# Optimization experiments

Hardware: AMD Instinct MI355X
Metric: run time of the kernel (lower is better)

## Reference

```python
import jax, jax.numpy as jnp
import numpy as np
from jax import lax

DN = ('NCHW', 'OIHW', 'NCHW')

def _conv(x, k, stride):
    return lax.conv_general_dilated(x, k, (stride, stride), 'VALID', dimension_numbers=DN)

def setup_inputs() -> dict:
    key = jax.random.key(0)
    ks = jax.random.split(key, 20)
    B, E, A, D = 2048, 8, 6, 64 * 7 * 7  # batch, rm_states, actions, flat conv dim (3136)
    s = 0.05
    inp = {
        'state': jax.random.normal(ks[0], (B, 84, 84, 3), jnp.float32),
        'rm_state': jax.random.randint(ks[1], (B,), 0, E, jnp.int64),
        # conv encoder params
        'k1': jax.random.normal(ks[2], (32, 3, 8, 8), jnp.float32) * s,
        'c1': jnp.zeros((32,), jnp.float32),
        'k2': jax.random.normal(ks[3], (64, 32, 4, 4), jnp.float32) * s,
        'c2': jnp.zeros((64,), jnp.float32),
        'k3': jax.random.normal(ks[4], (64, 64, 3, 3), jnp.float32) * s,
        'c3': jnp.zeros((64,), jnp.float32),
        # stacked per-rm-state expert MLP params (E experts)
        'W1': jax.random.normal(ks[5], (E, D, 64), jnp.float32) * s,
        'B1': jnp.zeros((E, 64), jnp.float32),
        'W2': jax.random.normal(ks[6], (E, 64, 64), jnp.float32) * s,
        'B2': jnp.zeros((E, 64), jnp.float32),
        'W3': jax.random.normal(ks[7], (E, 64, 64), jnp.float32) * s,
        'B3': jnp.zeros((E, 64), jnp.float32),
        'W4': jax.random.normal(ks[8], (E, 64, 64), jnp.float32) * s,
        'B4': jnp.zeros((E, 64), jnp.float32),
        'W5': jax.random.normal(ks[9], (E, 64, 64), jnp.float32) * s,
        'B5': jnp.zeros((E, 64), jnp.float32),
        'W6': jax.random.normal(ks[10], (E, 64, A), jnp.float32) * s,
        'B6': jnp.zeros((E, A), jnp.float32),
    }
    return inp

def reference(state, rm_state, k1, c1, k2, c2, k3, c3,
              W1, B1, W2, B2, W3, B3, W4, B4, W5, B5, W6, B6):
    # NHWC -> NCHW (matches torch's view-based channel-first rearrangement intent)
    x = jnp.transpose(state, (0, 3, 1, 2))
    x = jax.nn.relu(_conv(x, k1, 4) + c1[None, :, None, None])
    x = jax.nn.relu(_conv(x, k2, 2) + c2[None, :, None, None])
    x = jax.nn.relu(_conv(x, k3, 1) + c3[None, :, None, None])
    B = x.shape[0]
    flat = x.reshape(B, -1)                              # [B, 3136]
    # batched expert MLPs: compute all experts, then gather per-sample expert output
    h = jax.nn.relu(jnp.einsum('bd,edh->ebh', flat, W1) + B1[:, None, :])  # [E,B,64]
    for W, Bb in ((W2, B2), (W3, B3), (W4, B4), (W5, B5)):
        h = jax.nn.relu(jnp.einsum('ebh,ehk->ebk', h, W) + Bb[:, None, :])
    out = jnp.einsum('ebh,eha->eba', h, W6) + B6[:, None, :]               # [E,B,A]
    return out[rm_state, jnp.arange(B)]                  # [B, A]
```

## Files before the change

kernel.cpp:

```cpp
#include <hip/hip_runtime.h>

#define BATCH 2048

typedef unsigned short u16;
typedef __attribute__((ext_vector_type(8))) short bf16x8;
typedef __attribute__((ext_vector_type(4))) float f32x4;

static __device__ __forceinline__ float b2f(u16 h) {
  union { unsigned u; float f; } x; x.u = ((unsigned)h) << 16; return x.f;
}
static __device__ __forceinline__ u16 f2b(float f) {
  union { float f; unsigned u; } x; x.f = f;
  return (u16)((x.u + 0x7fffu + ((x.u >> 16) & 1u)) >> 16);
}
static __device__ __forceinline__ void split2(float v, u16& h, u16& l) {
  h = f2b(v); l = f2b(v - b2f(h));
}
static __device__ __forceinline__ bf16x8 ld8u(const u16* p, int idx) {
  union { bf16x8 v; ushort4 u[2]; } x;
  x.u[0] = *(const ushort4*)(p + idx);
  x.u[1] = *(const ushort4*)(p + idx + 4);
  return x.v;
}

__global__ void wsplit_kernel(const float* __restrict__ k1,
                              const float* __restrict__ k2,
                              const float* __restrict__ k3,
                              u16* __restrict__ W1d, u16* __restrict__ W2d,
                              u16* __restrict__ W3d)
{
  int id = blockIdx.x * 256 + threadIdx.x;
  float v; u16 *dh, *dl;
  if (id < 8192) {
    int ky = id >> 10, oc = (id >> 5) & 31, kk = id & 31;
    if (kk < 24) {
      int kx = kk / 3, c = kk - kx * 3;
      v = k1[oc * 192 + c * 64 + ky * 8 + kx];
    } else v = 0.f;
    dh = W1d + id; dl = W1d + 8192 + id;
  } else if (id < 40960) {
    int i = id - 8192;
    int pos = i >> 11, oc = (i >> 5) & 63, cc = i & 31;
    int ky = pos >> 2, kx = pos & 3;
    v = k2[oc * 512 + cc * 16 + ky * 4 + kx];
    dh = W2d + i; dl = W2d + 32768 + i;
  } else {
    int i = id - 40960;
    int j = i & 31, oc = (i >> 5) & 63, kc = (i >> 11) & 1, pos = i >> 12;
    int ky = pos / 3, kx = pos - ky * 3;
    v = k3[oc * 576 + (kc * 32 + j) * 9 + ky * 3 + kx];
    dh = W3d + i; dl = W3d + 36864 + i;
  }
  u16 h, l; split2(v, h, l); *dh = h; *dl = l;
}

__global__ void w1split_kernel(const float* __restrict__ W1,
                               u16* __restrict__ W1s)
{
  int id = blockIdx.x * 256 + threadIdx.x;
  int e = id / 200704;
  int r2 = id - e * 200704;
  int k = r2 >> 6, c = r2 & 63;
  float v = W1[id];
  u16 h, l; split2(v, h, l);
  int d = e * 200704 + (k >> 5) * 2048 + c * 32 + (k & 31);
  W1s[d] = h; W1s[1605632 + d] = l;
}

__global__ __launch_bounds__(512, 4) void conv_fused_kernel(
    const float* __restrict__ state, const u16* __restrict__ W1d,
    const u16* __restrict__ W2d, const u16* __restrict__ W3d,
    const float* __restrict__ c1, const float* __restrict__ c2,
    const float* __restrict__ c3, u16* __restrict__ a3h,
    u16* __restrict__ a3l)
{
  __shared__ __align__(16) u16 A1h[14400], A1l[14400];
  __shared__ __align__(16) u16 SHa[5832], SHb[5832];

  const int b = blockIdx.x, t = threadIdx.x;
  const int lane = t & 63, w = t >> 6, q = lane >> 4, n = lane & 15;

  for (int i = t; i < 792; i += 512) { SHa[5040 + i] = 0; SHb[5040 + i] = 0; }

  const int nT1 = (w < 2) ? 2 : 1;
  int pt1[2], ot1[2];
  if (w < 2) { pt1[0] = 0; ot1[0] = w; pt1[1] = 4; ot1[1] = w; }
  else       { pt1[0] = 1 + ((w - 2) >> 1); ot1[0] = (w - 2) & 1;
               pt1[1] = pt1[0]; ot1[1] = ot1[0]; }

  int aoff1[2];
  #pragma unroll
  for (int i = 0; i < 2; ++i) {
    int px = pt1[i] * 16 + n;
    int py = (px * 205) >> 12, pxx = px - py * 20;
    aoff1[i] = (py * 4) * 252 + pxx * 12 + q * 8;
  }
  float c1v[2];
  #pragma unroll
  for (int j = 0; j < 2; ++j) c1v[j] = c1[ot1[j] * 16 + n];
  const int ob1 = (ot1[0] * 16 + n) * 32 + q * 8;

  for (int by = 0; by < 5; ++by) {
    __syncthreads();
    const float4* sp = (const float4*)(state + (size_t)b * 21168 + by * 4032);
    #pragma unroll
    for (int pass = 0; pass < 3; ++pass) {
      int i = t + pass * 512;
      if (i < 1260) {
        float4 v = sp[i];
        u16 h0, l0, h1, l1, h2, l2, h3, l3;
        split2(v.x, h0, l0); split2(v.y, h1, l1);
        split2(v.z, h2, l2); split2(v.w, h3, l3);
        ushort4 hh; hh.x = h0; hh.y = h1; hh.z = h2; hh.w = h3;
        ushort4 ll; ll.x = l0; ll.y = l1; ll.z = l2; ll.w = l3;
        *(ushort4*)&SHa[i * 4] = hh;
        *(ushort4*)&SHb[i * 4] = ll;
      }
    }
    __syncthreads();

    f32x4 acc1[2] = {};
    bf16x8 bhc = *(const bf16x8*)(W1d + ob1);
    bf16x8 boc = *(const bf16x8*)(W1d + 8192 + ob1);
    for (int ky = 0; ky < 8; ++ky) {
      const int kyn = (ky < 7) ? ky + 1 : 7;
      bf16x8 bhn = *(const bf16x8*)(W1d + kyn * 1024 + ob1);
      bf16x8 bon = *(const bf16x8*)(W1d + 8192 + kyn * 1024 + ob1);
      #pragma unroll
      for (int i = 0; i < 2; ++i) if (i < nT1) {
        bf16x8 ah = ld8u(SHa, aoff1[i] + ky * 252);
        bf16x8 al = ld8u(SHb, aoff1[i] + ky * 252);
        acc1[i] = __builtin_amdgcn_mfma_f32_16x16x32_bf16(ah, bhc, acc1[i], 0, 0, 0);
        acc1[i] = __builtin_amdgcn_mfma_f32_16x16x32_bf16(ah, boc, acc1[i], 0, 0, 0);
        acc1[i] = __builtin_amdgcn_mfma_f32_16x16x32_bf16(al, bhc, acc1[i], 0, 0, 0);
      }
      bhc = bhn; boc = bon;
    }
    #pragma unroll
    for (int i = 0; i < 2; ++i) if (i < nT1) {
      int oc = ot1[i] * 16 + n;
      #pragma unroll
      for (int r = 0; r < 4; ++r) {
        int px = by * 80 + pt1[i] * 16 + q * 4 + r;
        float v = fmaxf(acc1[i][r] + c1v[i], 0.f);
        u16 h, l; split2(v, h, l);
        A1h[px * 36 + oc] = h; A1l[px * 36 + oc] = l;
      }
    }
  }
  __syncthreads();

  {
    const int ot2 = w & 3, pg2 = (w >> 2) * 3;
    int aoff2[3];
    #pragma unroll
    for (int i = 0; i < 3; ++i) {
      int px = (pg2 + i) * 16 + n; if (px > 80) px = 80;
      int py = (px * 7282) >> 16, pxx = px - py * 9;
      aoff2[i] = 2 * (py * 20 + pxx) * 36 + q * 8;
    }
    const float c2v = c2[ot2 * 16 + n];
    const int ob2 = (ot2 * 16 + n) * 32 + q * 8;

    f32x4 acc2[3] = {};
    bf16x8 bhc = *(const bf16x8*)(W2d + ob2);
    bf16x8 boc = *(const bf16x8*)(W2d + 32768 + ob2);
    for (int pos = 0; pos < 16; ++pos) {
      const int posn = (pos < 15) ? pos + 1 : 15;
      bf16x8 bhn = *(const bf16x8*)(W2d + posn * 2048 + ob2);
      bf16x8 bon = *(const bf16x8*)(W2d + 32768 + posn * 2048 + ob2);
      const int o = ((pos >> 2) * 20 + (pos & 3)) * 36;
      #pragma unroll
      for (int i = 0; i < 3; ++i) {
        bf16x8 ah = ld8u(A1h, aoff2[i] + o);
        bf16x8 al = ld8u(A1l, aoff2[i] + o);
        acc2[i] = __builtin_amdgcn_mfma_f32_16x16x32_bf16(ah, bhc, acc2[i], 0, 0, 0);
        acc2[i] = __builtin_amdgcn_mfma_f32_16x16x32_bf16(ah, boc, acc2[i], 0, 0, 0);
        acc2[i] = __builtin_amdgcn_mfma_f32_16x16x32_bf16(al, bhc, acc2[i], 0, 0, 0);
      }
      bhc = bhn; boc = bon;
    }
    #pragma unroll
    for (int i = 0; i < 3; ++i) {
      int oc = ot2 * 16 + n;
      #pragma unroll
      for (int r = 0; r < 4; ++r) {
        int px = (pg2 + i) * 16 + q * 4 + r;
        if (px < 81) {
          float v = fmaxf(acc2[i][r] + c2v, 0.f);
          u16 h, l; split2(v, h, l);
          SHa[px * 72 + oc] = h; SHb[px * 72 + oc] = l;
        }
      }
    }
  }
  __syncthreads();

  {
    const int ot3 = w & 3, pg3 = (w >> 2) * 2;
    int aoff3[2];
    #pragma unroll
    for (int i = 0; i < 2; ++i) {
      int px = (pg3 + i) * 16 + n; if (px > 48) px = 48;
      int py = (px * 74) >> 9, pxx = px - py * 7;
      aoff3[i] = (py * 9 + pxx) * 72 + q * 8;
    }
    const float c3v = c3[ot3 * 16 + n];
    const int ob3 = (ot3 * 16 + n) * 32 + q * 8;

    f32x4 acc3[2] = {};
    bf16x8 bhc = *(const bf16x8*)(W3d + ob3);
    bf16x8 boc = *(const bf16x8*)(W3d + 36864 + ob3);
    for (int pk = 0; pk < 18; ++pk) {
      const int pkn = (pk < 17) ? pk + 1 : 17;
      bf16x8 bhn = *(const bf16x8*)(W3d + pkn * 2048 + ob3);
      bf16x8 bon = *(const bf16x8*)(W3d + 36864 + pkn * 2048 + ob3);
      const int pos = pk >> 1, kc = pk & 1;
      const int ky = pos / 3, kx = pos - ky * 3;
      const int o = (ky * 9 + kx) * 72 + kc * 32;
      #pragma unroll
      for (int i = 0; i < 2; ++i) {
        bf16x8 ah = *(const bf16x8*)&SHa[aoff3[i] + o];
        bf16x8 al = *(const bf16x8*)&SHb[aoff3[i] + o];
        acc3[i] = __builtin_amdgcn_mfma_f32_16x16x32_bf16(ah, bhc, acc3[i], 0, 0, 0);
        acc3[i] = __builtin_amdgcn_mfma_f32_16x16x32_bf16(ah, boc, acc3[i], 0, 0, 0);
        acc3[i] = __builtin_amdgcn_mfma_f32_16x16x32_bf16(al, bhc, acc3[i], 0, 0, 0);
      }
      bhc = bhn; boc = bon;
    }
    u16* oph = a3h + (size_t)b * 3136;
    u16* opl = a3l + (size_t)b * 3136;
    #pragma unroll
    for (int i = 0; i < 2; ++i) {
      int oc = ot3 * 16 + n;
      #pragma unroll
      for (int r = 0; r < 4; ++r) {
        int px = (pg3 + i) * 16 + q * 4 + r;
        if (px < 49) {
          float v = fmaxf(acc3[i][r] + c3v, 0.f);
          u16 h, l; split2(v, h, l);
          oph[oc * 49 + px] = h; opl[oc * 49 + px] = l;
        }
      }
    }
  }
}

__global__ void group_kernel(const void* __restrict__ rmv,
                             int* __restrict__ counts, int* __restrict__ idxb)
{
  __shared__ int lcnt[8];
  __shared__ int isI32;
  const int t = threadIdx.x;
  if (t == 0) isI32 = 0;
  if (t < 8) lcnt[t] = 0;
  __syncthreads();
  unsigned long long v = ((const unsigned long long*)rmv)[t];
  if (v >= 8ull) isI32 = 1;
  __syncthreads();
  const int i32 = isI32;
  for (int b = t; b < BATCH; b += 1024) {
    int e = i32 ? ((const int*)rmv)[b] : (int)((const long long*)rmv)[b];
    int pos = atomicAdd(&lcnt[e], 1);
    idxb[e * BATCH + pos] = b;
  }
  __syncthreads();
  if (t < 8) counts[t] = lcnt[t];
}

__global__ __launch_bounds__(512, 2) void mlp_kernel(
    const u16* __restrict__ a3h, const u16* __restrict__ a3l,
    const int* __restrict__ counts, const int* __restrict__ idxb,
    const u16* __restrict__ W1s, const float* __restrict__ B1,
    const float* __restrict__ W2, const float* __restrict__ B2,
    const float* __restrict__ W3, const float* __restrict__ B3,
    const float* __restrict__ W4, const float* __restrict__ B4,
    const float* __restrict__ W5, const float* __restrict__ B5,
    const float* __restrict__ W6, const float* __restrict__ B6,
    float* __restrict__ out)
{
  __shared__ __align__(16) u16 Ah[2][2304], Al[2][2304];
  __shared__ __align__(16) float Wl[4096];
  __shared__ float bl[64];
  __shared__ float W6l[384];
  __shared__ float B6l[8];
  __shared__ __align__(16) float Ht0[64 * 68];
  __shared__ __align__(16) float Ht1[64 * 68];
  __shared__ int s_id[64];

  const int e  = blockIdx.x >> 5;
  const int tl = blockIdx.x & 31;
  const int cnt = counts[e];
  const int n0 = tl * 64;
  if (n0 >= cnt) return;
  const int m = min(64, cnt - n0);
  const int t = threadIdx.x;
  if (t < 64)  s_id[t] = idxb[e * BATCH + n0 + min(t, m - 1)];
  if (t < 384) W6l[t] = W6[e * 384 + t];
  if (t < 6)   B6l[t] = B6[e * 6 + t];
  __syncthreads();

  const int lane = t & 63, w = t >> 6, q = lane >> 4, n = lane & 15;
  const int mh = w >> 2, nt = w & 3;
  const u16* Wb = W1s + (size_t)e * 200704;

  const int sr = t >> 3, sub = t & 7, kp = sub & 3;
  const u16* srcp = (sub < 4) ? a3h : a3l;
  const size_t srow = (size_t)s_id[sr] * 3136;
  const int aro = mh * 32 + n;
  const int obase = (nt * 16 + n) * 32 + q * 8;

  f32x4 acc0 = {}, acc1 = {};
  {
    ushort4 v0 = *(const ushort4*)(srcp + srow + kp * 8);
    ushort4 v1 = *(const ushort4*)(srcp + srow + kp * 8 + 4);
    u16* dst = (sub < 4) ? Ah[0] : Al[0];
    *(ushort4*)&dst[sr * 36 + kp * 8]     = v0;
    *(ushort4*)&dst[sr * 36 + kp * 8 + 4] = v1;
  }
  bf16x8 bhc = *(const bf16x8*)(Wb + obase);
  bf16x8 boc = *(const bf16x8*)(Wb + 1605632 + obase);
  __syncthreads();

  for (int ch = 0; ch < 98; ++ch) {
    const int cur = ch & 1;
    if (ch < 97) {
      const int k0n = (ch + 1) * 32;
      ushort4 v0 = *(const ushort4*)(srcp + srow + k0n + kp * 8);
      ushort4 v1 = *(const ushort4*)(srcp + srow + k0n + kp * 8 + 4);
      u16* dst = (sub < 4) ? Ah[cur ^ 1] : Al[cur ^ 1];
      *(ushort4*)&dst[sr * 36 + kp * 8]     = v0;
      *(ushort4*)&dst[sr * 36 + kp * 8 + 4] = v1;
    }
    const int chn = (ch < 97) ? ch + 1 : 97;
    bf16x8 bhn = *(const bf16x8*)(Wb + chn * 2048 + obase);
    bf16x8 bon = *(const bf16x8*)(Wb + 1605632 + chn * 2048 + obase);

    bf16x8 a0h = ld8u(Ah[cur], aro * 36 + q * 8);
    bf16x8 a0l = ld8u(Al[cur], aro * 36 + q * 8);
    bf16x8 a1h = ld8u(Ah[cur], (aro + 16) * 36 + q * 8);
    bf16x8 a1l = ld8u(Al[cur], (aro + 16) * 36 + q * 8);
    acc0 = __builtin_amdgcn_mfma_f32_16x16x32_bf16(a0h, bhc, acc0, 0, 0, 0);
    acc0 = __builtin_amdgcn_mfma_f32_16x16x32_bf16(a0h, boc, acc0, 0, 0, 0);
    acc0 = __builtin_amdgcn_mfma_f32_16x16x32_bf16(a0l, bhc, acc0, 0, 0, 0);
    acc1 = __builtin_amdgcn_mfma_f32_16x16x32_bf16(a1h, bhc, acc1, 0, 0, 0);
    acc1 = __builtin_amdgcn_mfma_f32_16x16x32_bf16(a1h, boc, acc1, 0, 0, 0);
    acc1 = __builtin_amdgcn_mfma_f32_16x16x32_bf16(a1l, bhc, acc1, 0, 0, 0);
    bhc = bhn; boc = bon;
    __syncthreads();
  }

  {
    const int c = nt * 16 + n;
    const float b1v = B1[e * 64 + c];
    #pragma unroll
    for (int rr = 0; rr < 4; ++rr) {
      Ht0[c * 68 + mh * 32 + q * 4 + rr]      = fmaxf(acc0[rr] + b1v, 0.f);
      Ht0[c * 68 + mh * 32 + 16 + q * 4 + rr] = fmaxf(acc1[rr] + b1v, 0.f);
    }
  }

  const int tx = t & 15, ty = t >> 4;
  const int c0 = tx * 4, r0 = ty * 2;
  const float* Ws[4] = {W2, W3, W4, W5};
  const float* Bs[4] = {B2, B3, B4, B5};
  float* Hc = Ht0; float* Hn = Ht1;

  for (int L = 0; L < 4; ++L) {
    __syncthreads();
    const float* We = Ws[L] + (size_t)e * 4096;
    for (int i = t; i < 1024; i += 512)
      *(float4*)&Wl[i * 4] = *(const float4*)&We[i * 4];
    if (t < 64) bl[t] = Bs[L][e * 64 + t];
    __syncthreads();

    float acc[2][4] = {};
    #pragma unroll 4
    for (int kk = 0; kk < 64; ++kk) {
      float a0 = Hc[kk * 68 + r0], a1 = Hc[kk * 68 + r0 + 1];
      float4 bb = *(const float4*)&Wl[kk * 64 + c0];
      float bv[4] = {bb.x, bb.y, bb.z, bb.w};
      #pragma unroll
      for (int j = 0; j < 4; ++j) {
        acc[0][j] += a0 * bv[j];
        acc[1][j] += a1 * bv[j];
      }
    }
    __syncthreads();
    #pragma unroll
    for (int j = 0; j < 4; ++j) {
      float bias = bl[c0 + j];
      Hn[(c0 + j) * 68 + r0]     = fmaxf(acc[0][j] + bias, 0.f);
      Hn[(c0 + j) * 68 + r0 + 1] = fmaxf(acc[1][j] + bias, 0.f);
    }
    float* tmp = Hc; Hc = Hn; Hn = tmp;
  }
  __syncthreads();

  const int r = t & 63, aa = t >> 6;
  if (aa < 6) {
    float s = 0.f;
    for (int k = 0; k < 64; ++k)
      s += Hc[k * 68 + r] * W6l[k * 6 + aa];
    if (r < m) out[s_id[r] * 6 + aa] = s + B6l[aa];
  }
}

extern "C" void kernel_launch(void* const* d_in, const int* in_sizes, int n_in,
                              void* d_out, int out_size, void* d_ws, size_t ws_size,
                              hipStream_t stream) {
  const float* state = (const float*)d_in[0];
  const void*  rm    = d_in[1];
  const float* k1 = (const float*)d_in[2];
  const float* c1 = (const float*)d_in[3];
  const float* k2 = (const float*)d_in[4];
  const float* c2 = (const float*)d_in[5];
  const float* k3 = (const float*)d_in[6];
  const float* c3 = (const float*)d_in[7];
  const float* W1 = (const float*)d_in[8];
  const float* B1 = (const float*)d_in[9];
  const float* W2 = (const float*)d_in[10];
  const float* B2 = (const float*)d_in[11];
  const float* W3 = (const float*)d_in[12];
  const float* B3 = (const float*)d_in[13];
  const float* W4 = (const float*)d_in[14];
  const float* B4 = (const float*)d_in[15];
  const float* W5 = (const float*)d_in[16];
  const float* B5 = (const float*)d_in[17];
  const float* W6 = (const float*)d_in[18];
  const float* B6 = (const float*)d_in[19];

  char* ws = (char*)d_ws;
  u16* a3h    = (u16*)(ws);
  u16* a3l    = (u16*)(ws + 12845056);
  int* counts = (int*)(ws + 25690112);
  int* idxb   = (int*)(ws + 25690144);
  u16* W1d    = (u16*)(ws + 25755680);
  u16* W2d    = (u16*)(ws + 25788448);
  u16* W3d    = (u16*)(ws + 25919520);
  u16* W1s    = (u16*)(ws + 26066976);

  wsplit_kernel<<<304, 256, 0, stream>>>(k1, k2, k3, W1d, W2d, W3d);
  w1split_kernel<<<6272, 256, 0, stream>>>(W1, W1s);
  group_kernel<<<1, 1024, 0, stream>>>(rm, counts, idxb);

  conv_fused_kernel<<<2048, 512, 0, stream>>>(state, W1d, W2d, W3d,
                                              c1, c2, c3, a3h, a3l);

  mlp_kernel<<<256, 512, 0, stream>>>(a3h, a3l, counts, idxb, W1s, B1,
                                      W2, B2, W3, B3, W4, B4, W5, B5,
                                      W6, B6, (float*)d_out);
}
```

Before: 471.8 us.

## Halve MLP row tile, load A directly from global, vectorize W1 split

```diff
diff --git a/kernel.cpp b/kernel.cpp
--- a/kernel.cpp
+++ b/kernel.cpp
@@ -57,14 +57,26 @@
 __global__ void w1split_kernel(const float* __restrict__ W1,
                                u16* __restrict__ W1s)
 {
-  int id = blockIdx.x * 256 + threadIdx.x;
-  int e = id / 200704;
-  int r2 = id - e * 200704;
-  int k = r2 >> 6, c = r2 & 63;
-  float v = W1[id];
-  u16 h, l; split2(v, h, l);
-  int d = e * 200704 + (k >> 5) * 2048 + c * 32 + (k & 31);
-  W1s[d] = h; W1s[1605632 + d] = l;
+  const int bc = blockIdx.x;
+  const int e = bc / 98, chunk = bc - e * 98;
+  const int t = threadIdx.x;
+  const float* in = W1 + (size_t)e * 200704 + chunk * 2048;
+  const int c = t >> 2, kk0 = (t & 3) * 8;
+  u16 h[8], l[8];
+  #pragma unroll
+  for (int j = 0; j < 8; ++j) {
+    float v = in[(kk0 + j) * 64 + c];
+    split2(v, h[j], l[j]);
+  }
+  ushort4 h0; h0.x = h[0]; h0.y = h[1]; h0.z = h[2]; h0.w = h[3];
+  ushort4 h1; h1.x = h[4]; h1.y = h[5]; h1.z = h[6]; h1.w = h[7];
+  ushort4 l0; l0.x = l[0]; l0.y = l[1]; l0.z = l[2]; l0.w = l[3];
+  ushort4 l1; l1.x = l[4]; l1.y = l[5]; l1.z = l[6]; l1.w = l[7];
+  size_t d = (size_t)e * 200704 + chunk * 2048 + t * 8;
+  *(ushort4*)(W1s + d)     = h0;
+  *(ushort4*)(W1s + d + 4) = h1;
+  *(ushort4*)(W1s + 1605632 + d)     = l0;
+  *(ushort4*)(W1s + 1605632 + d + 4) = l1;
 }
 
 __global__ __launch_bounds__(512, 4) void conv_fused_kernel(
@@ -268,7 +280,7 @@
   if (t < 8) counts[t] = lcnt[t];
 }
 
-__global__ __launch_bounds__(512, 2) void mlp_kernel(
+__global__ __launch_bounds__(512, 4) void mlp_kernel(
     const u16* __restrict__ a3h, const u16* __restrict__ a3l,
     const int* __restrict__ counts, const int* __restrict__ idxb,
     const u16* __restrict__ W1s, const float* __restrict__ B1,
@@ -279,23 +291,22 @@
     const float* __restrict__ W6, const float* __restrict__ B6,
     float* __restrict__ out)
 {
-  __shared__ __align__(16) u16 Ah[2][2304], Al[2][2304];
+  __shared__ __align__(16) float Ht0[64 * 36];
+  __shared__ __align__(16) float Ht1[64 * 36];
   __shared__ __align__(16) float Wl[4096];
   __shared__ float bl[64];
   __shared__ float W6l[384];
   __shared__ float B6l[8];
-  __shared__ __align__(16) float Ht0[64 * 68];
-  __shared__ __align__(16) float Ht1[64 * 68];
-  __shared__ int s_id[64];
-
-  const int e  = blockIdx.x >> 5;
-  const int tl = blockIdx.x & 31;
+  __shared__ int s_id[32];
+
+  const int e  = blockIdx.x >> 6;
+  const int tl = blockIdx.x & 63;
   const int cnt = counts[e];
-  const int n0 = tl * 64;
+  const int n0 = tl * 32;
   if (n0 >= cnt) return;
-  const int m = min(64, cnt - n0);
+  const int m = min(32, cnt - n0);
   const int t = threadIdx.x;
-  if (t < 64)  s_id[t] = idxb[e * BATCH + n0 + min(t, m - 1)];
+  if (t < 32)  s_id[t] = idxb[e * BATCH + n0 + min(t, m - 1)];
   if (t < 384) W6l[t] = W6[e * 384 + t];
   if (t < 6)   B6l[t] = B6[e * 6 + t];
   __syncthreads();
@@ -303,65 +314,36 @@
   const int lane = t & 63, w = t >> 6, q = lane >> 4, n = lane & 15;
   const int mh = w >> 2, nt = w & 3;
   const u16* Wb = W1s + (size_t)e * 200704;
-
-  const int sr = t >> 3, sub = t & 7, kp = sub & 3;
-  const u16* srcp = (sub < 4) ? a3h : a3l;
-  const size_t srow = (size_t)s_id[sr] * 3136;
-  const int aro = mh * 32 + n;
+  const size_t srow = (size_t)s_id[mh * 16 + n] * 3136;
+  const int aoff = q * 8;
   const int obase = (nt * 16 + n) * 32 + q * 8;
 
-  f32x4 acc0 = {}, acc1 = {};
-  {
-    ushort4 v0 = *(const ushort4*)(srcp + srow + kp * 8);
-    ushort4 v1 = *(const ushort4*)(srcp + srow + kp * 8 + 4);
-    u16* dst = (sub < 4) ? Ah[0] : Al[0];
-    *(ushort4*)&dst[sr * 36 + kp * 8]     = v0;
-    *(ushort4*)&dst[sr * 36 + kp * 8 + 4] = v1;
-  }
+  f32x4 acc = {};
+  bf16x8 ahc = *(const bf16x8*)(a3h + srow + aoff);
+  bf16x8 alc = *(const bf16x8*)(a3l + srow + aoff);
   bf16x8 bhc = *(const bf16x8*)(Wb + obase);
   bf16x8 boc = *(const bf16x8*)(Wb + 1605632 + obase);
-  __syncthreads();
-
   for (int ch = 0; ch < 98; ++ch) {
-    const int cur = ch & 1;
-    if (ch < 97) {
-      const int k0n = (ch + 1) * 32;
-      ushort4 v0 = *(const ushort4*)(srcp + srow + k0n + kp * 8);
-      ushort4 v1 = *(const ushort4*)(srcp + srow + k0n + kp * 8 + 4);
-      u16* dst = (sub < 4) ? Ah[cur ^ 1] : Al[cur ^ 1];
-      *(ushort4*)&dst[sr * 36 + kp * 8]     = v0;
-      *(ushort4*)&dst[sr * 36 + kp * 8 + 4] = v1;
-    }
     const int chn = (ch < 97) ? ch + 1 : 97;
+    bf16x8 ahn = *(const bf16x8*)(a3h + srow + chn * 32 + aoff);
+    bf16x8 aln = *(const bf16x8*)(a3l + srow + chn * 32 + aoff);
     bf16x8 bhn = *(const bf16x8*)(Wb + chn * 2048 + obase);
     bf16x8 bon = *(const bf16x8*)(Wb + 1605632 + chn * 2048 + obase);
-
-    bf16x8 a0h = ld8u(Ah[cur], aro * 36 + q * 8);
-    bf16x8 a0l = ld8u(Al[cur], aro * 36 + q * 8);
-    bf16x8 a1h = ld8u(Ah[cur], (aro + 16) * 36 + q * 8);
-    bf16x8 a1l = ld8u(Al[cur], (aro + 16) * 36 + q * 8);
-    acc0 = __builtin_amdgcn_mfma_f32_16x16x32_bf16(a0h, bhc, acc0, 0, 0, 0);
-    acc0 = __builtin_amdgcn_mfma_f32_16x16x32_bf16(a0h, boc, acc0, 0, 0, 0);
-    acc0 = __builtin_amdgcn_mfma_f32_16x16x32_bf16(a0l, bhc, acc0, 0, 0, 0);
-    acc1 = __builtin_amdgcn_mfma_f32_16x16x32_bf16(a1h, bhc, acc1, 0, 0, 0);
-    acc1 = __builtin_amdgcn_mfma_f32_16x16x32_bf16(a1h, boc, acc1, 0, 0, 0);
-    acc1 = __builtin_amdgcn_mfma_f32_16x16x32_bf16(a1l, bhc, acc1, 0, 0, 0);
-    bhc = bhn; boc = bon;
-    __syncthreads();
+    acc = __builtin_amdgcn_mfma_f32_16x16x32_bf16(ahc, bhc, acc, 0, 0, 0);
+    acc = __builtin_amdgcn_mfma_f32_16x16x32_bf16(ahc, boc, acc, 0, 0, 0);
+    acc = __builtin_amdgcn_mfma_f32_16x16x32_bf16(alc, bhc, acc, 0, 0, 0);
+    ahc = ahn; alc = aln; bhc = bhn; boc = bon;
   }
 
   {
     const int c = nt * 16 + n;
     const float b1v = B1[e * 64 + c];
     #pragma unroll
-    for (int rr = 0; rr < 4; ++rr) {
-      Ht0[c * 68 + mh * 32 + q * 4 + rr]      = fmaxf(acc0[rr] + b1v, 0.f);
-      Ht0[c * 68 + mh * 32 + 16 + q * 4 + rr] = fmaxf(acc1[rr] + b1v, 0.f);
-    }
-  }
-
-  const int tx = t & 15, ty = t >> 4;
-  const int c0 = tx * 4, r0 = ty * 2;
+    for (int rr = 0; rr < 4; ++rr)
+      Ht0[c * 36 + mh * 16 + q * 4 + rr] = fmaxf(acc[rr] + b1v, 0.f);
+  }
+
+  const int r0 = t >> 4, c0 = (t & 15) * 4;
   const float* Ws[4] = {W2, W3, W4, W5};
   const float* Bs[4] = {B2, B3, B4, B5};
   float* Hc = Ht0; float* Hn = Ht1;
@@ -374,34 +356,27 @@
     if (t < 64) bl[t] = Bs[L][e * 64 + t];
     __syncthreads();
 
-    float acc[2][4] = {};
+    float acc4[4] = {};
     #pragma unroll 4
     for (int kk = 0; kk < 64; ++kk) {
-      float a0 = Hc[kk * 68 + r0], a1 = Hc[kk * 68 + r0 + 1];
+      float a = Hc[kk * 36 + r0];
       float4 bb = *(const float4*)&Wl[kk * 64 + c0];
-      float bv[4] = {bb.x, bb.y, bb.z, bb.w};
-      #pragma unroll
-      for (int j = 0; j < 4; ++j) {
-        acc[0][j] += a0 * bv[j];
-        acc[1][j] += a1 * bv[j];
-      }
+      acc4[0] += a * bb.x; acc4[1] += a * bb.y;
+      acc4[2] += a * bb.z; acc4[3] += a * bb.w;
     }
     __syncthreads();
     #pragma unroll
-    for (int j = 0; j < 4; ++j) {
-      float bias = bl[c0 + j];
-      Hn[(c0 + j) * 68 + r0]     = fmaxf(acc[0][j] + bias, 0.f);
-      Hn[(c0 + j) * 68 + r0 + 1] = fmaxf(acc[1][j] + bias, 0.f);
-    }
+    for (int j = 0; j < 4; ++j)
+      Hn[(c0 + j) * 36 + r0] = fmaxf(acc4[j] + bl[c0 + j], 0.f);
     float* tmp = Hc; Hc = Hn; Hn = tmp;
   }
   __syncthreads();
 
-  const int r = t & 63, aa = t >> 6;
+  const int r = t & 31, aa = t >> 5;
   if (aa < 6) {
     float s = 0.f;
     for (int k = 0; k < 64; ++k)
-      s += Hc[k * 68 + r] * W6l[k * 6 + aa];
+      s += Hc[k * 36 + r] * W6l[k * 6 + aa];
     if (r < m) out[s_id[r] * 6 + aa] = s + B6l[aa];
   }
 }
@@ -441,13 +416,13 @@
   u16* W1s    = (u16*)(ws + 26066976);
 
   wsplit_kernel<<<304, 256, 0, stream>>>(k1, k2, k3, W1d, W2d, W3d);
-  w1split_kernel<<<6272, 256, 0, stream>>>(W1, W1s);
+  w1split_kernel<<<784, 256, 0, stream>>>(W1, W1s);
   group_kernel<<<1, 1024, 0, stream>>>(rm, counts, idxb);
 
   conv_fused_kernel<<<2048, 512, 0, stream>>>(state, W1d, W2d, W3d,
                                               c1, c2, c3, a3h, a3l);
 
-  mlp_kernel<<<256, 512, 0, stream>>>(a3h, a3l, counts, idxb, W1s, B1,
+  mlp_kernel<<<512, 512, 0, stream>>>(a3h, a3l, counts, idxb, W1s, B1,
                                       W2, B2, W3, B3, W4, B4, W5, B5,
                                       W6, B6, (float*)d_out);
 }
```

After: 531.8 us. 12.7% more time.
